# Performance work log

Measured on AMD Instinct MI355X. Metric: run time of the kernel, lower is better.

## Reference

```python
import jax, jax.numpy as jnp
import numpy as np

WINDOW = 25  # causal sliding-window size for trend extraction


def setup_inputs() -> dict:
    key = jax.random.key(0)
    kx, kw1, kb1, kw2, kb2 = jax.random.split(key, 5)
    T = 720
    bound = 1.0 / np.sqrt(T)
    x = jax.random.normal(kx, (32, 512, T), dtype=jnp.float32)
    trend_w = jax.random.uniform(kw1, (T, T), jnp.float32, -bound, bound)
    trend_b = jax.random.uniform(kb1, (T,), jnp.float32, -bound, bound)
    seasonal_w = jax.random.uniform(kw2, (T, T), jnp.float32, -bound, bound)
    seasonal_b = jax.random.uniform(kb2, (T,), jnp.float32, -bound, bound)
    return {"x": x, "trend_w": trend_w, "trend_b": trend_b,
            "seasonal_w": seasonal_w, "seasonal_b": seasonal_b}


def _causal_window_mean(x, window):
    # x: [B, N, T]; trend[..., j] = mean(x[..., max(0, j-window+1):j+1])
    T = x.shape[-1]
    cs = jnp.cumsum(x, axis=-1)
    cs_shift = jnp.concatenate(
        [jnp.zeros(x.shape[:-1] + (window,), x.dtype), cs[..., :T - window]], axis=-1)
    counts = jnp.minimum(jnp.arange(T) + 1, window).astype(x.dtype)
    return (cs - cs_shift) / counts


def reference(x, trend_w, trend_b, seasonal_w, seasonal_b):
    trend = _causal_window_mean(x, WINDOW)
    seasonal = x - trend
    trend_out = jnp.einsum('bnt,ut->bnu', trend, trend_w) + trend_b
    seasonal_out = jnp.einsum('bnt,ut->bnu', seasonal, seasonal_w) + seasonal_b
    return trend_out + seasonal_out
```

## Files before the change

### kernel.cpp

```cpp
#include <hip/hip_runtime.h>
#include <hip/hip_bf16.h>


#define Tdim  720
#define KP    736
#define WROWS 768
#define NK    23
#define BM    64
#define APAD  740

using bf16x8 = __attribute__((ext_vector_type(8))) __bf16;
using f32x4  = __attribute__((ext_vector_type(4))) float;

__global__ void fold_w_kernel(const float* __restrict__ tw,
                              const float* __restrict__ tb,
                              const float* __restrict__ sw,
                              const float* __restrict__ sb,
                              __bf16* __restrict__ Wb,
                              float* __restrict__ beff) {
  int idx = blockIdx.x * 256 + threadIdx.x;
  if (idx >= WROWS * KP) return;
  int u = idx / KP;
  int i = idx - u * KP;
  float w = 0.0f;
  if (u < Tdim && i < Tdim) {
    const float* twr = tw + (size_t)u * Tdim;
    const float* swr = sw + (size_t)u * Tdim;
    int tend = (i + 25 < Tdim) ? (i + 25) : Tdim;
    float acc = 0.0f;
    if (i >= 24) {
      #pragma unroll 5
      for (int t = i; t < tend; ++t) acc += twr[t] - swr[t];
      acc *= 0.04f;
    } else {
      for (int t = i; t < tend; ++t) {
        float c = (t >= 24) ? 0.04f : 1.0f / (float)(t + 1);
        acc += (twr[t] - swr[t]) * c;
      }
    }
    w = swr[i] + acc;
  }
  Wb[idx] = (__bf16)w;
  if (i == 0 && u < Tdim) beff[u] = tb[u] + sb[u];
}

__global__ __launch_bounds__(512, 2)
void dlinear_gemm(const float* __restrict__ x,
                  const __bf16* __restrict__ Wb,
                  const float* __restrict__ beff,
                  float* __restrict__ out) {
  __shared__ __bf16 As[BM * APAD];

  const int tid  = threadIdx.x;
  const int lane = tid & 63;
  const int wid  = tid >> 6;
  const int lg = lane >> 4, lr = lane & 15;

  const int m0 = blockIdx.x * BM;
  const int u0 = wid * 96;

  #pragma unroll
  for (int c = 0; c < 12; ++c) {
    int idx = tid + 512 * c;
    if (idx < BM * 90) {
      int row  = idx / 90;
      int col8 = idx - row * 90;
      const float* p = x + (size_t)(m0 + row) * Tdim + col8 * 8;
      f32x4 a0 = ((const f32x4*)p)[0];
      f32x4 a1 = ((const f32x4*)p)[1];
      bf16x8 v;
      #pragma unroll
      for (int j = 0; j < 4; ++j) { v[j] = (__bf16)a0[j]; v[j + 4] = (__bf16)a1[j]; }
      *(bf16x8*)(&As[row * APAD + col8 * 8]) = v;
    }
  }
  {
    int r = tid >> 3;
    int c = 720 + (tid & 7) * 2;
    As[r * APAD + c]     = (__bf16)0.0f;
    As[r * APAD + c + 1] = (__bf16)0.0f;
  }
  __syncthreads();

  const __bf16* wp[6];
  #pragma unroll
  for (int ni = 0; ni < 6; ++ni)
    wp[ni] = Wb + (size_t)(u0 + ni * 16 + lr) * KP + lg * 8;

  int arofs[4];
  #pragma unroll
  for (int mi = 0; mi < 4; ++mi) arofs[mi] = (mi * 16 + lr) * APAD + lg * 8;

  f32x4 acc[4][6];
  #pragma unroll
  for (int mi = 0; mi < 4; ++mi)
    #pragma unroll
    for (int ni = 0; ni < 6; ++ni) {
      f32x4 z; z[0] = 0.f; z[1] = 0.f; z[2] = 0.f; z[3] = 0.f;
      acc[mi][ni] = z;
    }

  bf16x8 s0[6], s1[6], s2[6];
  #pragma unroll
  for (int ni = 0; ni < 6; ++ni) s0[ni] = *(const bf16x8*)(wp[ni]);
  #pragma unroll
  for (int ni = 0; ni < 6; ++ni) s1[ni] = *(const bf16x8*)(wp[ni] + 32);

#define GEMM_STEP(T, SLOT, ISSUE_SLOT, DO_ISSUE)                               \
  {                                                                            \
    if (DO_ISSUE) {                                                            \
      _Pragma("unroll")                                                        \
      for (int ni = 0; ni < 6; ++ni)                                           \
        ISSUE_SLOT[ni] = *(const bf16x8*)(wp[ni] + ((T) + 2) * 32);            \
    }                                                                          \
    bf16x8 av[4];                                                              \
    _Pragma("unroll")                                                          \
    for (int mi = 0; mi < 4; ++mi)                                             \
      av[mi] = *(const bf16x8*)(&As[arofs[mi] + (T) * 32]);                    \
    _Pragma("unroll")                                                          \
    for (int mi = 0; mi < 4; ++mi)                                             \
      _Pragma("unroll")                                                        \
      for (int ni = 0; ni < 6; ++ni)                                           \
        acc[mi][ni] = __builtin_amdgcn_mfma_f32_16x16x32_bf16(av[mi],          \
                        SLOT[ni], acc[mi][ni], 0, 0, 0);                       \
  }

  for (int t = 0; t < 21; t += 3) {
    GEMM_STEP(t,     s0, s2, true)
    GEMM_STEP(t + 1, s1, s0, true)
    GEMM_STEP(t + 2, s2, s1, true)
  }
  GEMM_STEP(21, s0, s2, false)
  GEMM_STEP(22, s1, s2, false)
#undef GEMM_STEP

  #pragma unroll
  for (int ni = 0; ni < 6; ++ni) {
    const int u = u0 + ni * 16 + lr;
    if (u >= Tdim) continue;
    const float bias = beff[u];
    #pragma unroll
    for (int mi = 0; mi < 4; ++mi) {
      const int mb = m0 + mi * 16 + lg * 4;
      #pragma unroll
      for (int j = 0; j < 4; ++j)
        out[(size_t)(mb + j) * Tdim + u] = acc[mi][ni][j] + bias;
    }
  }
}

extern "C" void kernel_launch(void* const* d_in, const int* in_sizes, int n_in,
                              void* d_out, int out_size, void* d_ws, size_t ws_size,
                              hipStream_t stream) {
  const float* x  = (const float*)d_in[0];
  const float* tw = (const float*)d_in[1];
  const float* tb = (const float*)d_in[2];
  const float* sw = (const float*)d_in[3];
  const float* sb = (const float*)d_in[4];
  float* out = (float*)d_out;

  __bf16* Wb  = (__bf16*)d_ws;
  float* beff = (float*)((char*)d_ws + (size_t)WROWS * KP * sizeof(__bf16));

  const int fold_total = WROWS * KP;
  fold_w_kernel<<<dim3((fold_total + 255) / 256), dim3(256), 0, stream>>>(
      tw, tb, sw, sb, Wb, beff);

  const int M = in_sizes[0] / Tdim;
  dim3 grid(M / BM);
  dlinear_gemm<<<grid, dim3(512), 0, stream>>>(x, Wb, beff, out);
}
```

Baseline: 46.81 us.

## Split warp N-tile into two passes to overlap stores and cut accumulator registers

Each wave now computes its 96 output columns as two sequential 48-column passes over K instead of one 96-column pass. This halves the accumulator and weight-prefetch register footprint and lets the first group's output stores overlap with the second group's K loop. The first weight fragments are also prefetched before the A-tile staging so global latency hides behind the LDS fill. In exchange, the A fragments in LDS are read twice and each pass issues fewer MFMAs per A load.

```diff
diff --git a/kernel.cpp b/kernel.cpp
--- a/kernel.cpp
+++ b/kernel.cpp
@@ -5,7 +5,6 @@
 #define Tdim  720
 #define KP    736
 #define WROWS 768
-#define NK    23
 #define BM    64
 #define APAD  740
 
@@ -59,6 +58,17 @@
   const int m0 = blockIdx.x * BM;
   const int u0 = wid * 96;
 
+  const __bf16* wp[6];
+  #pragma unroll
+  for (int ni = 0; ni < 6; ++ni)
+    wp[ni] = Wb + (size_t)(u0 + ni * 16 + lr) * KP + lg * 8;
+
+  bf16x8 s0[3], s1[3], s2[3];
+  #pragma unroll
+  for (int ni = 0; ni < 3; ++ni) s0[ni] = *(const bf16x8*)(wp[ni]);
+  #pragma unroll
+  for (int ni = 0; ni < 3; ++ni) s1[ni] = *(const bf16x8*)(wp[ni] + 32);
+
   #pragma unroll
   for (int c = 0; c < 12; ++c) {
     int idx = tid + 512 * c;
@@ -82,36 +92,18 @@
   }
   __syncthreads();
 
-  const __bf16* wp[6];
-  #pragma unroll
-  for (int ni = 0; ni < 6; ++ni)
-    wp[ni] = Wb + (size_t)(u0 + ni * 16 + lr) * KP + lg * 8;
-
   int arofs[4];
   #pragma unroll
   for (int mi = 0; mi < 4; ++mi) arofs[mi] = (mi * 16 + lr) * APAD + lg * 8;
 
-  f32x4 acc[4][6];
-  #pragma unroll
-  for (int mi = 0; mi < 4; ++mi)
-    #pragma unroll
-    for (int ni = 0; ni < 6; ++ni) {
-      f32x4 z; z[0] = 0.f; z[1] = 0.f; z[2] = 0.f; z[3] = 0.f;
-      acc[mi][ni] = z;
-    }
-
-  bf16x8 s0[6], s1[6], s2[6];
-  #pragma unroll
-  for (int ni = 0; ni < 6; ++ni) s0[ni] = *(const bf16x8*)(wp[ni]);
-  #pragma unroll
-  for (int ni = 0; ni < 6; ++ni) s1[ni] = *(const bf16x8*)(wp[ni] + 32);
-
-#define GEMM_STEP(T, SLOT, ISSUE_SLOT, DO_ISSUE)                               \
+  f32x4 acc[4][3];
+
+#define GEMM_STEP(T, GB, SLOT, ISSUE_SLOT, DO_ISSUE)                           \
   {                                                                            \
     if (DO_ISSUE) {                                                            \
       _Pragma("unroll")                                                        \
-      for (int ni = 0; ni < 6; ++ni)                                           \
-        ISSUE_SLOT[ni] = *(const bf16x8*)(wp[ni] + ((T) + 2) * 32);            \
+      for (int ni = 0; ni < 3; ++ni)                                           \
+        ISSUE_SLOT[ni] = *(const bf16x8*)(wp[(GB) + ni] + ((T) + 2) * 32);     \
     }                                                                          \
     bf16x8 av[4];                                                              \
     _Pragma("unroll")                                                          \
@@ -120,33 +112,72 @@
     _Pragma("unroll")                                                          \
     for (int mi = 0; mi < 4; ++mi)                                             \
       _Pragma("unroll")                                                        \
-      for (int ni = 0; ni < 6; ++ni)                                           \
+      for (int ni = 0; ni < 3; ++ni)                                           \
         acc[mi][ni] = __builtin_amdgcn_mfma_f32_16x16x32_bf16(av[mi],          \
                         SLOT[ni], acc[mi][ni], 0, 0, 0);                       \
   }
 
-  for (int t = 0; t < 21; t += 3) {
-    GEMM_STEP(t,     s0, s2, true)
-    GEMM_STEP(t + 1, s1, s0, true)
-    GEMM_STEP(t + 2, s2, s1, true)
-  }
-  GEMM_STEP(21, s0, s2, false)
-  GEMM_STEP(22, s1, s2, false)
+#define KLOOP(GB)                                                              \
+  for (int t = 0; t < 21; t += 3) {                                            \
+    GEMM_STEP(t,     GB, s0, s2, true)                                         \
+    GEMM_STEP(t + 1, GB, s1, s0, true)                                         \
+    GEMM_STEP(t + 2, GB, s2, s1, true)                                         \
+  }                                                                            \
+  GEMM_STEP(21, GB, s0, s2, false)                                             \
+  GEMM_STEP(22, GB, s1, s2, false)
+
+#define STORE_GROUP(GB)                                                        \
+  {                                                                            \
+    _Pragma("unroll")                                                          \
+    for (int ni = 0; ni < 3; ++ni) {                                           \
+      const int u = u0 + ((GB) + ni) * 16 + lr;                                \
+      if (u < Tdim) {                                                          \
+        const float bias = beff[u];                                            \
+        _Pragma("unroll")                                                      \
+        for (int mi = 0; mi < 4; ++mi) {                                       \
+          const int mb = m0 + mi * 16 + lg * 4;                                \
+          _Pragma("unroll")                                                    \
+          for (int j = 0; j < 4; ++j)                                          \
+            out[(size_t)(mb + j) * Tdim + u] = acc[mi][ni][j] + bias;          \
+        }                                                                      \
+      }                                                                        \
+    }                                                                          \
+  }
+
+  #pragma unroll
+  for (int mi = 0; mi < 4; ++mi)
+    #pragma unroll
+    for (int ni = 0; ni < 3; ++ni) {
+      f32x4 z; z[0] = 0.f; z[1] = 0.f; z[2] = 0.f; z[3] = 0.f;
+      acc[mi][ni] = z;
+    }
+  KLOOP(0)
+
+  bf16x8 n0a[3], n1a[3];
+  #pragma unroll
+  for (int ni = 0; ni < 3; ++ni) n0a[ni] = *(const bf16x8*)(wp[3 + ni]);
+  #pragma unroll
+  for (int ni = 0; ni < 3; ++ni) n1a[ni] = *(const bf16x8*)(wp[3 + ni] + 32);
+
+  STORE_GROUP(0)
+
+  #pragma unroll
+  for (int mi = 0; mi < 4; ++mi)
+    #pragma unroll
+    for (int ni = 0; ni < 3; ++ni) {
+      f32x4 z; z[0] = 0.f; z[1] = 0.f; z[2] = 0.f; z[3] = 0.f;
+      acc[mi][ni] = z;
+    }
+  #pragma unroll
+  for (int ni = 0; ni < 3; ++ni) s0[ni] = n0a[ni];
+  #pragma unroll
+  for (int ni = 0; ni < 3; ++ni) s1[ni] = n1a[ni];
+  KLOOP(3)
+  STORE_GROUP(3)
+
 #undef GEMM_STEP
-
-  #pragma unroll
-  for (int ni = 0; ni < 6; ++ni) {
-    const int u = u0 + ni * 16 + lr;
-    if (u >= Tdim) continue;
-    const float bias = beff[u];
-    #pragma unroll
-    for (int mi = 0; mi < 4; ++mi) {
-      const int mb = m0 + mi * 16 + lg * 4;
-      #pragma unroll
-      for (int j = 0; j < 4; ++j)
-        out[(size_t)(mb + j) * Tdim + u] = acc[mi][ni][j] + bias;
-    }
-  }
+#undef KLOOP
+#undef STORE_GROUP
 }
 
 extern "C" void kernel_launch(void* const* d_in, const int* in_sizes, int n_in,
```

After: 49.03 us. 1.05x slower.

## Pipeline A-tile loads in K chunks with double-buffered LDS

Applied to the files above, without the earlier changes.

Instead of loading the whole 64x720 activation tile into shared memory before any MFMA work, the kernel now stages x in 160-column chunks into two small LDS buffers. The next chunk's global loads are issued before the current chunk's MFMAs, then converted and written after them. This overlaps global-load latency with compute and cuts LDS use per block. The cost is extra barriers, register staging and more complex indexing, including zero-padding of the last chunk.

```diff
diff --git a/kernel.cpp b/kernel.cpp
--- a/kernel.cpp
+++ b/kernel.cpp
@@ -5,11 +5,11 @@
 #define Tdim  720
 #define KP    736
 #define WROWS 768
-#define NK    23
 #define BM    64
-#define APAD  740
+#define LSTR  164
 
 using bf16x8 = __attribute__((ext_vector_type(8))) __bf16;
+using bf16x4 = __attribute__((ext_vector_type(4))) __bf16;
 using f32x4  = __attribute__((ext_vector_type(4))) float;
 
 __global__ void fold_w_kernel(const float* __restrict__ tw,
@@ -49,7 +49,7 @@
                   const __bf16* __restrict__ Wb,
                   const float* __restrict__ beff,
                   float* __restrict__ out) {
-  __shared__ __bf16 As[BM * APAD];
+  __shared__ __bf16 As[2][BM * LSTR];
 
   const int tid  = threadIdx.x;
   const int lane = tid & 63;
@@ -59,37 +59,33 @@
   const int m0 = blockIdx.x * BM;
   const int u0 = wid * 96;
 
-  #pragma unroll
-  for (int c = 0; c < 12; ++c) {
-    int idx = tid + 512 * c;
-    if (idx < BM * 90) {
-      int row  = idx / 90;
-      int col8 = idx - row * 90;
-      const float* p = x + (size_t)(m0 + row) * Tdim + col8 * 8;
-      f32x4 a0 = ((const f32x4*)p)[0];
-      f32x4 a1 = ((const f32x4*)p)[1];
-      bf16x8 v;
-      #pragma unroll
-      for (int j = 0; j < 4; ++j) { v[j] = (__bf16)a0[j]; v[j + 4] = (__bf16)a1[j]; }
-      *(bf16x8*)(&As[row * APAD + col8 * 8]) = v;
-    }
-  }
-  {
-    int r = tid >> 3;
-    int c = 720 + (tid & 7) * 2;
-    As[r * APAD + c]     = (__bf16)0.0f;
-    As[r * APAD + c + 1] = (__bf16)0.0f;
-  }
-  __syncthreads();
-
   const __bf16* wp[6];
   #pragma unroll
   for (int ni = 0; ni < 6; ++ni)
     wp[ni] = Wb + (size_t)(u0 + ni * 16 + lr) * KP + lg * 8;
 
+  bf16x8 s0[6], s1[6], s2[6];
+  #pragma unroll
+  for (int ni = 0; ni < 6; ++ni) s0[ni] = *(const bf16x8*)(wp[ni]);
+  #pragma unroll
+  for (int ni = 0; ni < 6; ++ni) s1[ni] = *(const bf16x8*)(wp[ni] + 32);
+
+  #pragma unroll
+  for (int i = 0; i < 5; ++i) {
+    int unit = tid + 512 * i;
+    int row  = unit / 40;
+    int c4   = unit - row * 40;
+    f32x4 a = *(const f32x4*)(x + (size_t)(m0 + row) * Tdim + c4 * 4);
+    bf16x4 v;
+    #pragma unroll
+    for (int j = 0; j < 4; ++j) v[j] = (__bf16)a[j];
+    *(bf16x4*)(&As[0][row * LSTR + c4 * 4]) = v;
+  }
+  __syncthreads();
+
   int arofs[4];
   #pragma unroll
-  for (int mi = 0; mi < 4; ++mi) arofs[mi] = (mi * 16 + lr) * APAD + lg * 8;
+  for (int mi = 0; mi < 4; ++mi) arofs[mi] = (mi * 16 + lr) * LSTR + lg * 8;
 
   f32x4 acc[4][6];
   #pragma unroll
@@ -100,39 +96,115 @@
       acc[mi][ni] = z;
     }
 
-  bf16x8 s0[6], s1[6], s2[6];
-  #pragma unroll
-  for (int ni = 0; ni < 6; ++ni) s0[ni] = *(const bf16x8*)(wp[ni]);
-  #pragma unroll
-  for (int ni = 0; ni < 6; ++ni) s1[ni] = *(const bf16x8*)(wp[ni] + 32);
-
-#define GEMM_STEP(T, SLOT, ISSUE_SLOT, DO_ISSUE)                               \
-  {                                                                            \
-    if (DO_ISSUE) {                                                            \
+  f32x4 stg[5];
+
+#define STAGE_ISSUE_FULL(CB)                                                   \
+  { _Pragma("unroll")                                                          \
+    for (int i = 0; i < 5; ++i) {                                              \
+      int unit = tid + 512 * i;                                                \
+      int row  = unit / 40;                                                    \
+      int c4   = unit - row * 40;                                              \
+      stg[i] = *(const f32x4*)(x + (size_t)(m0 + row) * Tdim + (CB) + c4 * 4); \
+    } }
+
+#define STAGE_ISSUE_LAST()                                                     \
+  { _Pragma("unroll")                                                          \
+    for (int i = 0; i < 3; ++i) {                                              \
+      int unit = tid + 512 * i;                                                \
+      int row  = unit / 24;                                                    \
+      int c4   = unit - row * 24;                                              \
+      if (c4 < 20)                                                             \
+        stg[i] = *(const f32x4*)(x + (size_t)(m0 + row) * Tdim + 640 + c4 * 4);\
+      else { f32x4 z; z[0]=0.f; z[1]=0.f; z[2]=0.f; z[3]=0.f; stg[i] = z; }    \
+    } }
+
+#define STAGE_WRITE_FULL(BUF)                                                  \
+  { _Pragma("unroll")                                                          \
+    for (int i = 0; i < 5; ++i) {                                              \
+      int unit = tid + 512 * i;                                                \
+      int row  = unit / 40;                                                    \
+      int c4   = unit - row * 40;                                              \
+      bf16x4 v;                                                                \
+      _Pragma("unroll")                                                        \
+      for (int j = 0; j < 4; ++j) v[j] = (__bf16)stg[i][j];                    \
+      *(bf16x4*)(&As[BUF][row * LSTR + c4 * 4]) = v;                           \
+    } }
+
+#define STAGE_WRITE_LAST(BUF)                                                  \
+  { _Pragma("unroll")                                                          \
+    for (int i = 0; i < 3; ++i) {                                              \
+      int unit = tid + 512 * i;                                                \
+      int row  = unit / 24;                                                    \
+      int c4   = unit - row * 24;                                              \
+      bf16x4 v;                                                                \
+      _Pragma("unroll")                                                        \
+      for (int j = 0; j < 4; ++j) v[j] = (__bf16)stg[i][j];                    \
+      *(bf16x4*)(&As[BUF][row * LSTR + c4 * 4]) = v;                           \
+    } }
+
+#define KSTEP(G, TL, B, CUR, NXT, DO_LOAD)                                     \
+  { if (DO_LOAD) {                                                             \
       _Pragma("unroll")                                                        \
       for (int ni = 0; ni < 6; ++ni)                                           \
-        ISSUE_SLOT[ni] = *(const bf16x8*)(wp[ni] + ((T) + 2) * 32);            \
+        NXT[ni] = *(const bf16x8*)(wp[ni] + ((G) + 2) * 32);                   \
     }                                                                          \
     bf16x8 av[4];                                                              \
     _Pragma("unroll")                                                          \
     for (int mi = 0; mi < 4; ++mi)                                             \
-      av[mi] = *(const bf16x8*)(&As[arofs[mi] + (T) * 32]);                    \
+      av[mi] = *(const bf16x8*)(&As[B][arofs[mi] + (TL) * 32]);                \
     _Pragma("unroll")                                                          \
     for (int mi = 0; mi < 4; ++mi)                                             \
       _Pragma("unroll")                                                        \
       for (int ni = 0; ni < 6; ++ni)                                           \
         acc[mi][ni] = __builtin_amdgcn_mfma_f32_16x16x32_bf16(av[mi],          \
-                        SLOT[ni], acc[mi][ni], 0, 0, 0);                       \
-  }
-
-  for (int t = 0; t < 21; t += 3) {
-    GEMM_STEP(t,     s0, s2, true)
-    GEMM_STEP(t + 1, s1, s0, true)
-    GEMM_STEP(t + 2, s2, s1, true)
-  }
-  GEMM_STEP(21, s0, s2, false)
-  GEMM_STEP(22, s1, s2, false)
-#undef GEMM_STEP
+                        CUR[ni], acc[mi][ni], 0, 0, 0);                        \
+  }
+
+  STAGE_ISSUE_FULL(160)
+  KSTEP(0, 0, 0, s0, s2, true)
+  KSTEP(1, 1, 0, s1, s0, true)
+  KSTEP(2, 2, 0, s2, s1, true)
+  KSTEP(3, 3, 0, s0, s2, true)
+  KSTEP(4, 4, 0, s1, s0, true)
+  STAGE_WRITE_FULL(1)
+  __syncthreads();
+
+  STAGE_ISSUE_FULL(320)
+  KSTEP(5, 0, 1, s2, s1, true)
+  KSTEP(6, 1, 1, s0, s2, true)
+  KSTEP(7, 2, 1, s1, s0, true)
+  KSTEP(8, 3, 1, s2, s1, true)
+  KSTEP(9, 4, 1, s0, s2, true)
+  STAGE_WRITE_FULL(0)
+  __syncthreads();
+
+  STAGE_ISSUE_FULL(480)
+  KSTEP(10, 0, 0, s1, s0, true)
+  KSTEP(11, 1, 0, s2, s1, true)
+  KSTEP(12, 2, 0, s0, s2, true)
+  KSTEP(13, 3, 0, s1, s0, true)
+  KSTEP(14, 4, 0, s2, s1, true)
+  STAGE_WRITE_FULL(1)
+  __syncthreads();
+
+  STAGE_ISSUE_LAST()
+  KSTEP(15, 0, 1, s0, s2, true)
+  KSTEP(16, 1, 1, s1, s0, true)
+  KSTEP(17, 2, 1, s2, s1, true)
+  KSTEP(18, 3, 1, s0, s2, true)
+  KSTEP(19, 4, 1, s1, s0, true)
+  STAGE_WRITE_LAST(0)
+  __syncthreads();
+
+  KSTEP(20, 0, 0, s2, s1, true)
+  KSTEP(21, 1, 0, s0, s2, false)
+  KSTEP(22, 2, 0, s1, s2, false)
+
+#undef KSTEP
+#undef STAGE_ISSUE_FULL
+#undef STAGE_ISSUE_LAST
+#undef STAGE_WRITE_FULL
+#undef STAGE_WRITE_LAST
 
   #pragma unroll
   for (int ni = 0; ni < 6; ++ni) {
```

Result: slower. 49.64 us (+6.0%).
